# Optimization experiments

Measured on AMD Instinct MI355X. Metric: run time of the kernel, lower is better.

## Reference

```python
import jax, jax.numpy as jnp
import numpy as np

N_QUBITS = 12
N_LAYERS = 6
BATCH = 2048
N_OUTPUTS = 2
C64 = jnp.complex64


def setup_inputs() -> dict:
    key = jax.random.key(0)
    k1, k2 = jax.random.split(key)
    x = jax.random.normal(k1, (BATCH, N_QUBITS), dtype=jnp.float32)
    # nn.Parameter: torch.randn(n_layers, n_qubits, 3) * 0.1
    weights = jax.random.normal(k2, (N_LAYERS, N_QUBITS, 3), dtype=jnp.float32) * 0.1
    return {"x": x, "weights": weights}


def _rx(t):
    # t: (...,) angles -> (..., 2, 2) RX matrices
    c = jnp.cos(t * 0.5).astype(C64)
    s = (-1j * jnp.sin(t * 0.5)).astype(C64)
    return jnp.stack([jnp.stack([c, s], -1), jnp.stack([s, c], -1)], -2)


def _ry(t):
    c = jnp.cos(t * 0.5).astype(C64)
    s = jnp.sin(t * 0.5).astype(C64)
    return jnp.stack([jnp.stack([c, -s], -1), jnp.stack([s, c], -1)], -2)


def _rz(t):
    e = jnp.exp(-0.5j * t).astype(C64)
    z = jnp.zeros_like(e)
    return jnp.stack([jnp.stack([e, z], -1), jnp.stack([z, jnp.conj(e)], -1)], -2)


def _rot(w):
    # PennyLane Rot(phi, theta, omega) = RZ(omega) @ RY(theta) @ RZ(phi); w: (n_qubits, 3)
    return _rz(w[:, 2]) @ _ry(w[:, 1]) @ _rz(w[:, 0])


def _apply_1q(state, gate, q):
    # state: (B, 2**n) complex; gate: (2,2) or (B,2,2); qubit q (wire 0 = MSB)
    B = state.shape[0]
    s = state.reshape(B, 2 ** q, 2, -1)
    if gate.ndim == 3:
        s = jnp.einsum('bij,bljr->blir', gate, s)
    else:
        s = jnp.einsum('ij,bljr->blir', gate, s)
    return s.reshape(B, -1)


def _apply_cnot(state, c, t, n):
    # control c, target t; flip target axis where control bit == 1
    B = state.shape[0]
    s = state.reshape((B,) + (2,) * n)
    ac, at = 1 + c, 1 + t
    s0 = jnp.take(s, 0, axis=ac)
    s1 = jnp.take(s, 1, axis=ac)
    at2 = at - 1 if at > ac else at
    s1 = jnp.flip(s1, axis=at2)
    s = jnp.stack([s0, s1], axis=ac)
    return s.reshape(B, -1)


def _layer(state, w, n):
    # strongly-entangling layer: Rot on every wire, then full CNOT entanglement
    rot = _rot(w)  # (n, 2, 2)
    for q in range(n):
        state = _apply_1q(state, rot[q], q)
    for i in range(n):
        for j in range(i + 1, n):
            state = _apply_cnot(state, i, j, n)
    return state


def _forward(x, weights):
    n = N_QUBITS
    B = x.shape[0]
    state = jnp.zeros((B, 2 ** n), C64).at[:, 0].set(1.0)
    # angle encoding: RX(x_q) on wire q (PennyLane AngleEmbedding default axis X)
    for q in range(n):
        state = _apply_1q(state, _rx(x[:, q]), q)
    layer_ckpt = jax.checkpoint(lambda s, w: _layer(s, w, n))
    for l in range(N_LAYERS):
        state = layer_ckpt(state, weights[l])
    # expval(PauliZ) on wires 0..n_outputs-1
    probs = state.real ** 2 + state.imag ** 2  # (B, 2**n)
    outs = []
    for k in range(N_OUTPUTS):
        p = probs.reshape(B, 2 ** k, 2, -1)
        outs.append(p[:, :, 0, :].sum((1, 2)) - p[:, :, 1, :].sum((1, 2)))
    return jnp.stack(outs, -1)  # (B, n_outputs)


def reference(x, weights):
    return _forward(x, weights)
```

## Files before the change

### kernel.cpp

```cpp
#include <hip/hip_runtime.h>
#include <math.h>

#define NQ 12
#define DIM 4096
#define NL 6
#define TPB 256


#define WS_WA0 0
#define WS_W   512
#define WS_ZA0 3072
#define WS_ZM  3104
#define WS_RYT 3424
#define WS_FLOATS 3712

typedef float f2 __attribute__((ext_vector_type(2)));

__device__ __forceinline__ f2 pk_mul(f2 a, f2 b) {
  f2 d; asm("v_pk_mul_f32 %0, %1, %2" : "=v"(d) : "v"(a), "v"(b)); return d;
}
__device__ __forceinline__ f2 pk_fma(f2 a, f2 b, f2 c) {
  f2 d; asm("v_pk_fma_f32 %0, %1, %2, %3" : "=v"(d) : "v"(a), "v"(b), "v"(c)); return d;
}
__device__ __forceinline__ f2 cmulp(f2 a, f2 c) {
  f2 r1, d;
  asm("v_pk_mul_f32 %0, %1, %2 op_sel:[0,0] op_sel_hi:[0,1]"
      : "=v"(r1) : "v"(a), "v"(c));
  asm("v_pk_fma_f32 %0, %1, %2, %3 op_sel:[1,1,0] op_sel_hi:[1,0,1] neg_lo:[1,0,0]"
      : "=v"(d) : "v"(a), "v"(c), "v"(r1));
  return d;
}

template<int BIT>
__device__ __forceinline__ void apply_ry16(f2 v[16], f2 ww, f2 ss) {
  #pragma unroll
  for (int j = 0; j < 16; ++j) {
    if (j & (1 << BIT)) continue;
    const int k = j | (1 << BIT);
    f2 a = v[j], b = v[k];
    a = pk_fma(b, ww, a);
    b = pk_fma(a, ss, b);
    a = pk_fma(b, ww, a);
    v[j] = a; v[k] = b;
  }
}

__global__ __launch_bounds__(256)
void qprep_kernel(const float* __restrict__ w, float* __restrict__ ws) {
  const int t = threadIdx.x;

  {
    float f = 0.f;
    #pragma unroll
    for (int k = 0; k < 8; ++k) {
      float p = w[(0*NQ + 7 - k)*3 + 0];
      f += ((t >> k) & 1) ? 0.5f*p : -0.5f*p;
    }
    float sv, cv; sincosf(f, &sv, &cv);
    ws[WS_WA0 + 2*t] = cv; ws[WS_WA0 + 2*t + 1] = sv;
  }

  #pragma unroll 1
  for (int l = 0; l < NL-1; ++l) {
    float f = 0.f;
    const int gt = t ^ (t >> 1);
    #pragma unroll
    for (int k = 0; k < 8; ++k) {
      float om = w[(l*NQ + 11 - k)*3 + 2];
      f += ((t >> k) & 1) ? 0.5f*om : -0.5f*om;
    }
    #pragma unroll
    for (int k = 0; k < 7; ++k) {
      float ph = w[((l+1)*NQ + 11 - k)*3 + 0];
      f += ((gt >> k) & 1) ? 0.5f*ph : -0.5f*ph;
    }
    float sv, cv; sincosf(f, &sv, &cv);
    ws[WS_W + (l*256 + t)*2] = cv; ws[WS_W + (l*256 + t)*2 + 1] = sv;
  }

  if (t < 16) {
    float f = 0.f;
    #pragma unroll
    for (int m = 0; m < 4; ++m) {
      float p = w[(0*NQ + 11 - m)*3 + 0];
      f += ((t >> m) & 1) ? 0.5f*p : -0.5f*p;
    }
    float sv, cv; sincosf(f, &sv, &cv);
    ws[WS_ZA0 + 2*t] = cv; ws[WS_ZA0 + 2*t + 1] = sv;
  }

  if (t < 160) {
    const int l = t >> 5, h = (t >> 4) & 1, j = t & 15;
    float f = 0.f;
    #pragma unroll
    for (int m = 0; m < 4; ++m) {
      float om = w[(l*NQ + 3 - m)*3 + 2];
      f += ((j >> m) & 1) ? 0.5f*om : -0.5f*om;
    }
    {
      float p4 = w[((l+1)*NQ + 4)*3 + 0];
      f += (h ^ (j & 1)) ? 0.5f*p4 : -0.5f*p4;
    }
    const int gj = j ^ (j >> 1);
    #pragma unroll
    for (int m = 0; m < 4; ++m) {
      float ph = w[((l+1)*NQ + 3 - m)*3 + 0];
      f += ((gj >> m) & 1) ? 0.5f*ph : -0.5f*ph;
    }
    float sv, cv; sincosf(f, &sv, &cv);
    ws[WS_ZM + 2*t] = cv; ws[WS_ZM + 2*t + 1] = sv;
  }

  if (t < NL*NQ) {
    float th = w[t*3 + 1];
    float sv = sinf(0.5f*th);
    float wv = -tanf(0.25f*th);
    ((float4*)(ws + WS_RYT))[t] = make_float4(wv, wv, sv, sv);
  }
}

__global__ __launch_bounds__(TPB, 5)
void qsim12_kernel(const float* __restrict__ x, const float* __restrict__ ws,
                   float* __restrict__ out) {
  __shared__ __align__(16) float st[2*DIM];

  const int t = threadIdx.x;
  const int b = blockIdx.x;
  char* stb = (char*)st;

  float csx[NQ], csy[NQ];
  {
    const int q = t & 63;
    float xv = (q < NQ) ? x[b*NQ + q] : 0.f;
    float sv, cv; sincosf(0.5f*xv, &sv, &cv);
    #pragma unroll
    for (int qq = 0; qq < NQ; ++qq) {
      csx[qq] = __int_as_float(__builtin_amdgcn_readlane(__float_as_int(cv), qq));
      csy[qq] = __int_as_float(__builtin_amdgcn_readlane(__float_as_int(sv), qq));
    }
  }

  int baseA[8], baseB[8];
  #pragma unroll
  for (int m = 0; m < 8; ++m) {
    baseA[m] = (t << 7) + (((2*m) ^ (t & 14)) << 3);
    baseB[m] = ((t >> 4) << 11) + ((((t & 15) ^ (2*m))) << 3);
  }
  const int baseC = ((t >> 4) << 7) + ((((t & 15) ^ ((t >> 4) & 15))) << 3);
  const int G = t ^ (t >> 1);
  int baseS[2];
  #pragma unroll
  for (int par = 0; par < 2; ++par) {
    const int k8 = par << 3;
    baseS[par] = ((((G >> 4) & 15) ^ k8) << 7)
               + ((((G & 15) ^ ((G >> 4) & 14) ^ k8)) << 3);
  }

  f2 v[16];

  {
    float rhi = 1.f;
    #pragma unroll
    for (int k = 0; k < 8; ++k)
      rhi *= ((t >> k) & 1) ? csy[7-k] : csx[7-k];
    const int popt = __popc(t);
    #pragma unroll
    for (int j = 0; j < 16; ++j) {
      float r = rhi;
      #pragma unroll
      for (int m = 0; m < 4; ++m)
        r *= ((j >> m) & 1) ? csy[11-m] : csx[11-m];
      const int pj = (popt + __popc(j)) & 3;
      if      (pj == 0) v[j] = (f2){ r, 0.f};
      else if (pj == 1) v[j] = (f2){0.f, -r};
      else if (pj == 2) v[j] = (f2){-r, 0.f};
      else              v[j] = (f2){0.f,  r};
    }
  }

  #define RY(BIT, WQ)                                                     \
    { const float4 r = *(const float4*)(ws + WS_RYT + 4*(l*NQ + (WQ)));   \
      apply_ry16<BIT>(v, (f2){r.x, r.y}, (f2){r.z, r.w}); }

  #pragma unroll 1
  for (int l = 0; l < NL; ++l) {
    if (l > 0) {
      #pragma unroll
      for (int m = 0; m < 8; ++m) {
        float4 q4 = *(const float4*)(stb + baseA[m]);
        v[2*m]   = (f2){q4.x, q4.y};
        v[2*m+1] = (f2){q4.z, q4.w};
      }
    } else {
      const float2 wv = *(const float2*)(ws + WS_WA0 + 2*t);
      const f2 wA0 = (f2){wv.x, wv.y};
      #pragma unroll
      for (int j = 0; j < 16; ++j) {
        const float2 zv = *(const float2*)(ws + WS_ZA0 + 2*j);
        v[j] = cmulp(cmulp(v[j], (f2){zv.x, zv.y}), wA0);
      }
    }
    RY(0,11) RY(1,10) RY(2,9) RY(3,8)
    #pragma unroll
    for (int m = 0; m < 8; ++m)
      *(float4*)(stb + baseA[m]) =
          make_float4(v[2*m].x, v[2*m].y, v[2*m+1].x, v[2*m+1].y);
    __syncthreads();

    #pragma unroll
    for (int m = 0; m < 8; ++m) {
      v[2*m]   = *(const f2*)(stb + baseB[m] + (2*m)*128);
      v[2*m+1] = *(const f2*)(stb + baseB[m] + (2*m+1)*128);
    }
    RY(0,7) RY(1,6) RY(2,5) RY(3,4)
    #pragma unroll
    for (int m = 0; m < 8; ++m) {
      *(f2*)(stb + baseB[m] + (2*m)*128)         = v[2*m];
      *(f2*)(stb + (baseB[m] ^ 8) + (2*m+1)*128) = v[2*m+1];
    }
    __syncthreads();

    #pragma unroll
    for (int j = 0; j < 16; ++j)
      v[j] = *(const f2*)(stb + baseC + j*2048);
    RY(0,3) RY(1,2) RY(2,1) RY(3,0)
    if (l < NL-1) {
      const float2 wv = *(const float2*)(ws + WS_W + (l*TPB + t)*2);
      const f2 W = (f2){wv.x, wv.y};
      const float* zmb = ws + WS_ZM + ((l*2 + ((t >> 7) & 1))*16)*2;
      #pragma unroll
      for (int j = 0; j < 16; ++j) {
        const float2 zv = *(const float2*)(zmb + 2*j);
        v[j] = cmulp(cmulp(v[j], (f2){zv.x, zv.y}), W);
      }
      #pragma unroll
      for (int j = 0; j < 16; ++j) {
        const int g4 = (j ^ (j >> 1)) & 15;
        *(f2*)(stb + baseS[j & 1] + (g4 << 11)) = v[j];
      }
      __syncthreads();
    }
  }

  float a0 = 0.f, a1 = 0.f;
  #pragma unroll
  for (int j = 0; j < 16; ++j) {
    float pr = v[j].x*v[j].x + v[j].y*v[j].y;
    a0 += ((j >> 3) & 1) ? -pr : pr;
    a1 += (((j >> 2) ^ (j >> 3)) & 1) ? -pr : pr;
  }
  #pragma unroll
  for (int off = 32; off >= 1; off >>= 1) {
    a0 += __shfl_down(a0, off);
    a1 += __shfl_down(a1, off);
  }
  __syncthreads();
  if ((t & 63) == 0) { st[(t >> 6)*2] = a0; st[(t >> 6)*2 + 1] = a1; }
  __syncthreads();
  if (t == 0) {
    out[b*2 + 0] = st[0] + st[2] + st[4] + st[6];
    out[b*2 + 1] = st[1] + st[3] + st[5] + st[7];
  }
}

extern "C" void kernel_launch(void* const* d_in, const int* in_sizes, int n_in,
                              void* d_out, int out_size, void* d_ws, size_t ws_size,
                              hipStream_t stream) {
  const float* x = (const float*)d_in[0];
  const float* w = (const float*)d_in[1];
  float* out = (float*)d_out;
  float* ws = (float*)d_ws;
  int B = in_sizes[0] / NQ;
  qprep_kernel<<<1, 256, 0, stream>>>(w, ws);
  qsim12_kernel<<<B, TPB, 0, stream>>>(x, ws, out);
}
```

Before: 125.1 us.

## Process two batch elements per block with interleaved state vectors

Each block now simulates two batch elements, keeping two 16-amplitude register sets and two shared-memory state buffers. The two independent computations are interleaved between barriers so each barrier and the per-pass coefficient loads are shared across two statevectors, giving more instruction-level parallelism per wave. Shared memory per block doubles to 64KB, register pressure roughly doubles, and launch bounds drop to one block per SM hint, so occupancy falls. The launch assumes an even batch size.

```diff
diff --git a/kernel.cpp b/kernel.cpp
--- a/kernel.cpp
+++ b/kernel.cpp
@@ -119,26 +119,108 @@
   }
 }
 
-__global__ __launch_bounds__(TPB, 5)
+#define RYV(V, BIT, WQ) {                                                  \
+    const float4 r_ = *(const float4*)(ws + WS_RYT + 4*(l*NQ + (WQ)));     \
+    apply_ry16<BIT>(V, (f2){r_.x, r_.y}, (f2){r_.z, r_.w}); }
+
+#define PA_LOAD(V, STB)                                                    \
+  _Pragma("unroll")                                                        \
+  for (int m = 0; m < 8; ++m) {                                            \
+    float4 q4 = *(const float4*)((STB) + baseA[m]);                        \
+    V[2*m]   = (f2){q4.x, q4.y};                                           \
+    V[2*m+1] = (f2){q4.z, q4.w};                                           \
+  }
+
+#define PA_DIAG0(V) {                                                      \
+    const float2 wv_ = *(const float2*)(ws + WS_WA0 + 2*t);                \
+    const f2 wA0 = (f2){wv_.x, wv_.y};                                     \
+    _Pragma("unroll")                                                      \
+    for (int j = 0; j < 16; ++j) {                                         \
+      const float2 zv = *(const float2*)(ws + WS_ZA0 + 2*j);               \
+      V[j] = cmulp(cmulp(V[j], (f2){zv.x, zv.y}), wA0);                    \
+    } }
+
+#define PA_RY_STORE(V, STB)                                                \
+  RYV(V,0,11) RYV(V,1,10) RYV(V,2,9) RYV(V,3,8)                            \
+  _Pragma("unroll")                                                        \
+  for (int m = 0; m < 8; ++m)                                              \
+    *(float4*)((STB) + baseA[m]) =                                         \
+        make_float4(V[2*m].x, V[2*m].y, V[2*m+1].x, V[2*m+1].y);
+
+#define PB_LOAD(V, STB)                                                    \
+  _Pragma("unroll")                                                        \
+  for (int m = 0; m < 8; ++m) {                                            \
+    V[2*m]   = *(const f2*)((STB) + baseB[m] + (2*m)*128);                 \
+    V[2*m+1] = *(const f2*)((STB) + baseB[m] + (2*m+1)*128);               \
+  }
+
+#define PB_RY_STORE(V, STB)                                                \
+  RYV(V,0,7) RYV(V,1,6) RYV(V,2,5) RYV(V,3,4)                              \
+  _Pragma("unroll")                                                        \
+  for (int m = 0; m < 8; ++m) {                                            \
+    *(f2*)((STB) + baseB[m] + (2*m)*128)         = V[2*m];                 \
+    *(f2*)((STB) + (baseB[m] ^ 8) + (2*m+1)*128) = V[2*m+1];               \
+  }
+
+#define PC_LOAD(V, STB)                                                    \
+  _Pragma("unroll")                                                        \
+  for (int j = 0; j < 16; ++j)                                             \
+    V[j] = *(const f2*)((STB) + baseC + j*2048);
+
+#define PC_RY(V) RYV(V,0,3) RYV(V,1,2) RYV(V,2,1) RYV(V,3,0)
+
+#define PC_DIAG_FOLD(V, STB) {                                             \
+    const float2 wv_ = *(const float2*)(ws + WS_W + (l*TPB + t)*2);        \
+    const f2 W = (f2){wv_.x, wv_.y};                                       \
+    const float* zmb = ws + WS_ZM + ((l*2 + ((t >> 7) & 1))*16)*2;         \
+    _Pragma("unroll")                                                      \
+    for (int j = 0; j < 16; ++j) {                                         \
+      const float2 zv = *(const float2*)(zmb + 2*j);                       \
+      V[j] = cmulp(cmulp(V[j], (f2){zv.x, zv.y}), W);                      \
+    }                                                                      \
+    _Pragma("unroll")                                                      \
+    for (int j = 0; j < 16; ++j) {                                         \
+      const int g4 = (j ^ (j >> 1)) & 15;                                  \
+      *(f2*)((STB) + baseS[j & 1] + (g4 << 11)) = V[j];                    \
+    } }
+
+#define INIT_STATE(V, ELEM) {                                              \
+    float csx[NQ], csy[NQ];                                                \
+    const int q_ = t & 63;                                                 \
+    float xv = (q_ < NQ) ? x[(ELEM)*NQ + q_] : 0.f;                        \
+    float sv_, cv_; sincosf(0.5f*xv, &sv_, &cv_);                          \
+    _Pragma("unroll")                                                      \
+    for (int qq = 0; qq < NQ; ++qq) {                                      \
+      csx[qq] = __int_as_float(__builtin_amdgcn_readlane(__float_as_int(cv_), qq)); \
+      csy[qq] = __int_as_float(__builtin_amdgcn_readlane(__float_as_int(sv_), qq)); \
+    }                                                                      \
+    float rhi = 1.f;                                                       \
+    _Pragma("unroll")                                                      \
+    for (int k = 0; k < 8; ++k)                                            \
+      rhi *= ((t >> k) & 1) ? csy[7-k] : csx[7-k];                         \
+    const int popt = __popc(t);                                            \
+    _Pragma("unroll")                                                      \
+    for (int j = 0; j < 16; ++j) {                                         \
+      float r = rhi;                                                       \
+      _Pragma("unroll")                                                    \
+      for (int m = 0; m < 4; ++m)                                          \
+        r *= ((j >> m) & 1) ? csy[11-m] : csx[11-m];                       \
+      const int pj = (popt + __popc(j)) & 3;                               \
+      if      (pj == 0) V[j] = (f2){ r, 0.f};                              \
+      else if (pj == 1) V[j] = (f2){0.f, -r};                              \
+      else if (pj == 2) V[j] = (f2){-r, 0.f};                              \
+      else              V[j] = (f2){0.f,  r};                              \
+    } }
+
+__global__ __launch_bounds__(TPB, 1)
 void qsim12_kernel(const float* __restrict__ x, const float* __restrict__ ws,
                    float* __restrict__ out) {
-  __shared__ __align__(16) float st[2*DIM];
+  __shared__ __align__(16) float st[2][2*DIM];
 
   const int t = threadIdx.x;
-  const int b = blockIdx.x;
-  char* stb = (char*)st;
-
-  float csx[NQ], csy[NQ];
-  {
-    const int q = t & 63;
-    float xv = (q < NQ) ? x[b*NQ + q] : 0.f;
-    float sv, cv; sincosf(0.5f*xv, &sv, &cv);
-    #pragma unroll
-    for (int qq = 0; qq < NQ; ++qq) {
-      csx[qq] = __int_as_float(__builtin_amdgcn_readlane(__float_as_int(cv), qq));
-      csy[qq] = __int_as_float(__builtin_amdgcn_readlane(__float_as_int(sv), qq));
-    }
-  }
+  const int e0 = blockIdx.x*2, e1 = e0 + 1;
+  char* stbX = (char*)&st[0][0];
+  char* stbY = (char*)&st[1][0];
 
   int baseA[8], baseB[8];
   #pragma unroll
@@ -156,110 +238,69 @@
                + ((((G & 15) ^ ((G >> 4) & 14) ^ k8)) << 3);
   }
 
-  f2 v[16];
-
-  {
-    float rhi = 1.f;
-    #pragma unroll
-    for (int k = 0; k < 8; ++k)
-      rhi *= ((t >> k) & 1) ? csy[7-k] : csx[7-k];
-    const int popt = __popc(t);
-    #pragma unroll
-    for (int j = 0; j < 16; ++j) {
-      float r = rhi;
-      #pragma unroll
-      for (int m = 0; m < 4; ++m)
-        r *= ((j >> m) & 1) ? csy[11-m] : csx[11-m];
-      const int pj = (popt + __popc(j)) & 3;
-      if      (pj == 0) v[j] = (f2){ r, 0.f};
-      else if (pj == 1) v[j] = (f2){0.f, -r};
-      else if (pj == 2) v[j] = (f2){-r, 0.f};
-      else              v[j] = (f2){0.f,  r};
-    }
-  }
-
-  #define RY(BIT, WQ)                                                     \
-    { const float4 r = *(const float4*)(ws + WS_RYT + 4*(l*NQ + (WQ)));   \
-      apply_ry16<BIT>(v, (f2){r.x, r.y}, (f2){r.z, r.w}); }
+  f2 vX[16], vY[16];
+  INIT_STATE(vX, e0)
+  INIT_STATE(vY, e1)
 
   #pragma unroll 1
   for (int l = 0; l < NL; ++l) {
     if (l > 0) {
-      #pragma unroll
-      for (int m = 0; m < 8; ++m) {
-        float4 q4 = *(const float4*)(stb + baseA[m]);
-        v[2*m]   = (f2){q4.x, q4.y};
-        v[2*m+1] = (f2){q4.z, q4.w};
-      }
+      PA_LOAD(vX, stbX)
+      PA_LOAD(vY, stbY)
     } else {
-      const float2 wv = *(const float2*)(ws + WS_WA0 + 2*t);
-      const f2 wA0 = (f2){wv.x, wv.y};
-      #pragma unroll
-      for (int j = 0; j < 16; ++j) {
-        const float2 zv = *(const float2*)(ws + WS_ZA0 + 2*j);
-        v[j] = cmulp(cmulp(v[j], (f2){zv.x, zv.y}), wA0);
-      }
-    }
-    RY(0,11) RY(1,10) RY(2,9) RY(3,8)
-    #pragma unroll
-    for (int m = 0; m < 8; ++m)
-      *(float4*)(stb + baseA[m]) =
-          make_float4(v[2*m].x, v[2*m].y, v[2*m+1].x, v[2*m+1].y);
+      PA_DIAG0(vX)
+      PA_DIAG0(vY)
+    }
+    PA_RY_STORE(vX, stbX)
+    PA_RY_STORE(vY, stbY)
     __syncthreads();
 
-    #pragma unroll
-    for (int m = 0; m < 8; ++m) {
-      v[2*m]   = *(const f2*)(stb + baseB[m] + (2*m)*128);
-      v[2*m+1] = *(const f2*)(stb + baseB[m] + (2*m+1)*128);
-    }
-    RY(0,7) RY(1,6) RY(2,5) RY(3,4)
-    #pragma unroll
-    for (int m = 0; m < 8; ++m) {
-      *(f2*)(stb + baseB[m] + (2*m)*128)         = v[2*m];
-      *(f2*)(stb + (baseB[m] ^ 8) + (2*m+1)*128) = v[2*m+1];
-    }
+    PB_LOAD(vX, stbX)
+    PB_LOAD(vY, stbY)
+    PB_RY_STORE(vX, stbX)
+    PB_RY_STORE(vY, stbY)
     __syncthreads();
 
-    #pragma unroll
-    for (int j = 0; j < 16; ++j)
-      v[j] = *(const f2*)(stb + baseC + j*2048);
-    RY(0,3) RY(1,2) RY(2,1) RY(3,0)
+    PC_LOAD(vX, stbX)
+    PC_LOAD(vY, stbY)
+    PC_RY(vX)
+    PC_RY(vY)
     if (l < NL-1) {
-      const float2 wv = *(const float2*)(ws + WS_W + (l*TPB + t)*2);
-      const f2 W = (f2){wv.x, wv.y};
-      const float* zmb = ws + WS_ZM + ((l*2 + ((t >> 7) & 1))*16)*2;
-      #pragma unroll
-      for (int j = 0; j < 16; ++j) {
-        const float2 zv = *(const float2*)(zmb + 2*j);
-        v[j] = cmulp(cmulp(v[j], (f2){zv.x, zv.y}), W);
-      }
-      #pragma unroll
-      for (int j = 0; j < 16; ++j) {
-        const int g4 = (j ^ (j >> 1)) & 15;
-        *(f2*)(stb + baseS[j & 1] + (g4 << 11)) = v[j];
-      }
+      PC_DIAG_FOLD(vX, stbX)
+      PC_DIAG_FOLD(vY, stbY)
       __syncthreads();
     }
   }
 
-  float a0 = 0.f, a1 = 0.f;
+  float a0X = 0.f, a1X = 0.f, a0Y = 0.f, a1Y = 0.f;
   #pragma unroll
   for (int j = 0; j < 16; ++j) {
-    float pr = v[j].x*v[j].x + v[j].y*v[j].y;
-    a0 += ((j >> 3) & 1) ? -pr : pr;
-    a1 += (((j >> 2) ^ (j >> 3)) & 1) ? -pr : pr;
+    float prX = vX[j].x*vX[j].x + vX[j].y*vX[j].y;
+    float prY = vY[j].x*vY[j].x + vY[j].y*vY[j].y;
+    const float s0 = ((j >> 3) & 1) ? -1.f : 1.f;
+    const float s1 = (((j >> 2) ^ (j >> 3)) & 1) ? -1.f : 1.f;
+    a0X += s0*prX; a1X += s1*prX;
+    a0Y += s0*prY; a1Y += s1*prY;
   }
   #pragma unroll
   for (int off = 32; off >= 1; off >>= 1) {
-    a0 += __shfl_down(a0, off);
-    a1 += __shfl_down(a1, off);
+    a0X += __shfl_down(a0X, off);
+    a1X += __shfl_down(a1X, off);
+    a0Y += __shfl_down(a0Y, off);
+    a1Y += __shfl_down(a1Y, off);
   }
   __syncthreads();
-  if ((t & 63) == 0) { st[(t >> 6)*2] = a0; st[(t >> 6)*2 + 1] = a1; }
+  if ((t & 63) == 0) {
+    const int wv = t >> 6;
+    st[0][wv*2] = a0X; st[0][wv*2 + 1] = a1X;
+    st[1][wv*2] = a0Y; st[1][wv*2 + 1] = a1Y;
+  }
   __syncthreads();
   if (t == 0) {
-    out[b*2 + 0] = st[0] + st[2] + st[4] + st[6];
-    out[b*2 + 1] = st[1] + st[3] + st[5] + st[7];
+    out[e0*2 + 0] = st[0][0] + st[0][2] + st[0][4] + st[0][6];
+    out[e0*2 + 1] = st[0][1] + st[0][3] + st[0][5] + st[0][7];
+    out[e1*2 + 0] = st[1][0] + st[1][2] + st[1][4] + st[1][6];
+    out[e1*2 + 1] = st[1][1] + st[1][3] + st[1][5] + st[1][7];
   }
 }
 
@@ -272,5 +313,5 @@
   float* ws = (float*)d_ws;
   int B = in_sizes[0] / NQ;
   qprep_kernel<<<1, 256, 0, stream>>>(w, ws);
-  qsim12_kernel<<<B, TPB, 0, stream>>>(x, ws, out);
-}
+  qsim12_kernel<<<B/2, TPB, 0, stream>>>(x, ws, out);
+}
```

Result: slower. 135.2 us (+8.1%).
